# Kernel tuning notes

Measured on AMD Instinct MI355X. Metric: run time of the kernel, lower is better.

Reference implementation:

```python
import jax, jax.numpy as jnp
import numpy as np

B, L, D, H = 2, 2048, 2048, 16
Dh = D // H
EPS = 1e-6
THETA = 500000.0


def _rope_cos_sin(dh, seq_len):
    # matches init_rope: per-head dim, theta=500000
    inv_freqs = 1.0 / (THETA ** (jnp.arange(0, dh, 2, dtype=jnp.float32) / dh))  # [Dh/2]
    t = jnp.arange(seq_len, dtype=jnp.float32)
    freqs = jnp.outer(t, inv_freqs)  # [L, Dh/2]
    return jnp.cos(freqs), jnp.sin(freqs)


def _apply_rope(x, cos, sin):
    # x: [B,L,H,Dh]; cos/sin: [L,Dh/2]
    xr = x.reshape(*x.shape[:-1], -1, 2)  # [B,L,H,Dh/2,2]
    c = cos[None, :, None, :]
    s = sin[None, :, None, :]
    rot = jnp.stack([xr[..., 0] * c - xr[..., 1] * s,
                     xr[..., 1] * c + xr[..., 0] * s], axis=-1)
    return rot.reshape(x.shape)


def setup_inputs() -> dict:
    key = jax.random.key(0)
    ks = jax.random.split(key, 5)
    std = 0.02
    x = jax.random.normal(ks[0], (B, L, D), dtype=jnp.float32)
    Wq = std * jax.random.normal(ks[1], (D, H, Dh), dtype=jnp.float32)
    Wk = std * jax.random.normal(ks[2], (D, H, Dh), dtype=jnp.float32)
    Wv = std * jax.random.normal(ks[3], (D, H, Dh), dtype=jnp.float32)
    Wout = (std / jnp.sqrt(2.0 * 24)) * jax.random.normal(ks[4], (D, D), dtype=jnp.float32)
    attn_scale = jnp.asarray(jnp.log2(float(L) ** 2 - float(L)), dtype=jnp.float32)
    return {"x": x, "Wq": Wq, "Wk": Wk, "Wv": Wv, "Wout": Wout, "attn_scale": attn_scale}


def reference(x, Wq, Wk, Wv, Wout, attn_scale):
    cos, sin = _rope_cos_sin(Dh, L)
    q = jnp.einsum('bld,dhk->blhk', x, Wq)  # [B,L,H,Dh]
    k = jnp.einsum('bld,dhk->blhk', x, Wk)
    v = jnp.einsum('bld,dhk->blhk', x, Wv)
    q = _apply_rope(q, cos, sin)
    k = _apply_rope(k, cos, sin)
    # QK L2 normalization
    q = q / (jnp.linalg.norm(q, axis=-1, keepdims=True) + EPS)
    k = k / (jnp.linalg.norm(k, axis=-1, keepdims=True) + EPS)
    att = jnp.einsum('bqhd,bkhd->bhqk', q, k)  # [B,H,L,L]
    mask = jnp.tril(jnp.ones((1, 1, L, L), dtype=jnp.bool_))
    neg_inf = jnp.finfo(jnp.float32).min
    att = jnp.where(mask, att, neg_inf)
    att = attn_scale * att
    att = jax.nn.softmax(att, axis=-1)
    out = jnp.einsum('bhqk,bkhd->bqhd', att, v)  # [B,L,H,Dh]
    out = out.reshape(B, L, D)
    return jnp.einsum('bld,de->ble', out, Wout)
```

## Files before the change

kernel.cpp:

```cpp
#include <hip/hip_runtime.h>
#include <hip/hip_fp16.h>

#define B_ 2
#define L_ 2048
#define D_ 2048
#define H_ 16
#define DH_ 128

typedef _Float16 f16;
typedef _Float16 f16x8 __attribute__((ext_vector_type(8)));
typedef _Float16 f16x4 __attribute__((ext_vector_type(4)));
typedef _Float16 f16x2 __attribute__((ext_vector_type(2)));
typedef float f32x4 __attribute__((ext_vector_type(4)));

__device__ __forceinline__ void gload_lds16(const void* g, void* l) {
  __builtin_amdgcn_global_load_lds(
      (__attribute__((address_space(1))) void*)(void*)g,
      (__attribute__((address_space(3))) void*)l, 16, 0, 0);
}

template <int N>
__device__ __forceinline__ void waitcnt_vm() {
  if constexpr (N == 0) asm volatile("s_waitcnt vmcnt(0)" ::: "memory");
  else if constexpr (N == 4) asm volatile("s_waitcnt vmcnt(4)" ::: "memory");
  else if constexpr (N == 6) asm volatile("s_waitcnt vmcnt(6)" ::: "memory");
  else if constexpr (N == 8) asm volatile("s_waitcnt vmcnt(8)" ::: "memory");
}

__device__ __forceinline__ float rmax16(float v) {
  v = fmaxf(v, __shfl_xor(v, 1));
  v = fmaxf(v, __shfl_xor(v, 2));
  v = fmaxf(v, __shfl_xor(v, 4));
  v = fmaxf(v, __shfl_xor(v, 8));
  return v;
}
__device__ __forceinline__ float rsum16(float v) {
  v += __shfl_xor(v, 1);
  v += __shfl_xor(v, 2);
  v += __shfl_xor(v, 4);
  v += __shfl_xor(v, 8);
  return v;
}

__global__ __launch_bounds__(256) void k_cast(const float* __restrict__ in,
                                              f16* __restrict__ out, int n8) {
  int i = blockIdx.x * blockDim.x + threadIdx.x;
  if (i >= n8) return;
  const float4* p = (const float4*)in + (size_t)i * 2;
  float4 a = p[0], b = p[1];
  f16x8 o;
  o[0] = (f16)a.x; o[1] = (f16)a.y; o[2] = (f16)a.z; o[3] = (f16)a.w;
  o[4] = (f16)b.x; o[5] = (f16)b.y; o[6] = (f16)b.z; o[7] = (f16)b.w;
  *((f16x8*)out + i) = o;
}

__global__ __launch_bounds__(256) void k_transpose4(
    const float* __restrict__ W0, const float* __restrict__ W1,
    const float* __restrict__ W2, const float* __restrict__ W3,
    f16* __restrict__ T0, f16* __restrict__ T1, f16* __restrict__ T2,
    f16* __restrict__ T3) {
  int z = blockIdx.z;
  const float* src = (z == 0) ? W0 : (z == 1) ? W1 : (z == 2) ? W2 : W3;
  f16* dst = (z == 0) ? T0 : (z == 1) ? T1 : (z == 2) ? T2 : T3;
  __shared__ float tile[32][33];
  int tx = threadIdx.x, ty = threadIdx.y;
  int x = blockIdx.x * 32 + tx;
  int y0 = blockIdx.y * 32;
#pragma unroll
  for (int i = 0; i < 4; ++i)
    tile[ty + i * 8][tx] = src[(size_t)(y0 + ty + i * 8) * 2048 + x];
  __syncthreads();
  int ox = y0 + tx;
  int oy0 = blockIdx.x * 32;
#pragma unroll
  for (int i = 0; i < 4; ++i)
    dst[(size_t)(oy0 + ty + i * 8) * 2048 + ox] = (f16)tile[tx][ty + i * 8];
}


template <int NL>
__device__ __forceinline__ void stage_slot(const char* __restrict__ src,
                                           char* dst, int tid) {
#pragma unroll
  for (int j = 0; j < NL; ++j) {
    int ci = j * 512 + tid;
    int row = ci >> 3;
    int sc = (ci & 7) ^ (row & 7);
    gload_lds16(src + (size_t)row * 4096 + sc * 16, dst + ci * 16);
  }
}

template <int BM>
__device__ __forceinline__ void gemm8_core(const f16* __restrict__ A,
                                           const f16* __restrict__ BT,
                                           char* lds, int m0, int n0,
                                           f32x4 (&acc)[BM / 32][4]) {
  constexpr int WRS = BM / 2;
  constexpr int MR = BM / 32;
  constexpr int MPP = MR / 4;
  constexpr int ALOADS = BM / 128;
  constexpr int LPT = 2 * ALOADS + 4;
  constexpr int ABYTES = BM * 128;
  constexpr int BUFB = ABYTES + 32768;
  constexpr int nt = 32;

  const int tid = threadIdx.x;
  const int lane = tid & 63, w = tid >> 6;
  const int wr = w >> 2, wc = w & 3;
  const int li = lane & 15, lg = lane >> 4;

  const char* Ab = (const char*)A + (size_t)m0 * 4096;
  const char* Bb = (const char*)BT + (size_t)n0 * 4096;

  const int aoff0 = (wr * WRS + li) * 128 + ((lg) ^ (li & 7)) * 16;
  const int aoff1 = (wr * WRS + li) * 128 + ((4 + lg) ^ (li & 7)) * 16;
  const int boff0 = (wc * 64 + li) * 128 + ((lg) ^ (li & 7)) * 16;
  const int boff1 = (wc * 64 + li) * 128 + ((4 + lg) ^ (li & 7)) * 16;

#pragma unroll
  for (int t = 0; t < 2; ++t) {
    char* bA = lds + t * BUFB;
    stage_slot<ALOADS>(Ab + t * 128, bA, tid);
    stage_slot<ALOADS>(Ab + (size_t)WRS * 4096 + t * 128, bA + (size_t)WRS * 128, tid);
    stage_slot<2>(Bb + t * 128, bA + ABYTES, tid);
    stage_slot<2>(Bb + (size_t)128 * 4096 + t * 128, bA + ABYTES + 128 * 128, tid);
  }
  waitcnt_vm<LPT>();
  __builtin_amdgcn_s_barrier();

#pragma unroll 1
  for (int u = 0; u < nt; ++u) {
    const int c = u & 1;
    char* bufA = lds + c * BUFB;
    char* bufB = bufA + ABYTES;
    char* oA = lds + (c ^ 1) * BUFB;
    f16x8 bf[4][2];
#pragma unroll
    for (int p = 0; p < 4; ++p) {
      f16x8 af[MPP][2];
#pragma unroll
      for (int i = 0; i < MPP; ++i) {
        af[i][0] = *(const f16x8*)(bufA + aoff0 + (p * MPP + i) * 2048);
        af[i][1] = *(const f16x8*)(bufA + aoff1 + (p * MPP + i) * 2048);
      }
      if (p == 0) {
#pragma unroll
        for (int nc = 0; nc < 4; ++nc) {
          bf[nc][0] = *(const f16x8*)(bufB + boff0 + nc * 2048);
          bf[nc][1] = *(const f16x8*)(bufB + boff1 + nc * 2048);
        }
      }
      if (p == 0 && u >= 1 && u + 1 < nt)
        stage_slot<ALOADS>(Ab + (size_t)(u + 1) * 128, oA, tid);
      if (p == 1 && u >= 1 && u + 1 < nt)
        stage_slot<ALOADS>(Ab + (size_t)WRS * 4096 + (size_t)(u + 1) * 128,
                           oA + (size_t)WRS * 128, tid);
      if (p == 2 && u + 2 < nt)
        stage_slot<2>(Bb + (size_t)(u + 2) * 128, bufB, tid);
      if (p == 3 && u + 2 < nt)
        stage_slot<2>(Bb + (size_t)128 * 4096 + (size_t)(u + 2) * 128,
                      bufB + 128 * 128, tid);
      if (p == 3) {
        if (u + 2 < nt) waitcnt_vm<4>();
        else if (u + 1 < nt) waitcnt_vm<0>();
      }
      __builtin_amdgcn_s_barrier();
      asm volatile("s_waitcnt lgkmcnt(0)" ::: "memory");
      __builtin_amdgcn_sched_barrier(0);
      __builtin_amdgcn_s_setprio(1);
#pragma unroll
      for (int i = 0; i < MPP; ++i)
#pragma unroll
        for (int nc = 0; nc < 4; ++nc) {
          acc[p * MPP + i][nc] = __builtin_amdgcn_mfma_f32_16x16x32_f16(
              af[i][0], bf[nc][0], acc[p * MPP + i][nc], 0, 0, 0);
          acc[p * MPP + i][nc] = __builtin_amdgcn_mfma_f32_16x16x32_f16(
              af[i][1], bf[nc][1], acc[p * MPP + i][nc], 0, 0, 0);
        }
      __builtin_amdgcn_s_setprio(0);
      __builtin_amdgcn_s_barrier();
    }
  }
}

__global__ __launch_bounds__(512, 2) void k_gemm8_qkv(
    const f16* __restrict__ x16, const f16* __restrict__ WqT,
    const f16* __restrict__ WkT, const f16* __restrict__ WvT,
    f16* __restrict__ qh, f16* __restrict__ kh, f16* __restrict__ vTo) {
  __shared__ alignas(16) char lds[2 * (256 * 128 + 32768)];
  const int pb = blockIdx.x;
  const int lgc = (pb & 7) * 48 + (pb >> 3);
  const int z = lgc >> 7;
  const int r = lgc & 127;
  const int m0 = (r >> 3) * 256, n0 = (r & 7) * 256;
  const f16* BT = (z == 0) ? WqT : (z == 1) ? WkT : WvT;
  f32x4 acc[8][4] = {};
  gemm8_core<256>(x16, BT, lds, m0, n0, acc);

  const int lane = threadIdx.x & 63, w = threadIdx.x >> 6;
  const int wr = w >> 2, wc = w & 3, li = lane & 15, lg = lane >> 4;
  if (z < 2) {
    f16* out = (z == 0) ? qh : kh;
#pragma unroll
    for (int mr = 0; mr < 8; ++mr) {
      int mb = m0 + wr * 128 + mr * 16 + lg * 4;
#pragma unroll
      for (int nc = 0; nc < 4; ++nc) {
        int n = n0 + wc * 64 + nc * 16 + li;
        int h = n >> 7, dh = n & 127;
#pragma unroll
        for (int r2 = 0; r2 < 4; ++r2) {
          int m = mb + r2;
          int b = m >> 11, l = m & 2047;
          out[(((size_t)(b * 16 + h) * 2048 + l) << 7) + dh] = (f16)acc[mr][nc][r2];
        }
      }
    }
  } else {
#pragma unroll
    for (int mr = 0; mr < 8; ++mr) {
      int mb = m0 + wr * 128 + mr * 16 + lg * 4;
      int b = mb >> 11, l = mb & 2047;
#pragma unroll
      for (int nc = 0; nc < 4; ++nc) {
        int n = n0 + wc * 64 + nc * 16 + li;
        int h = n >> 7, dh = n & 127;
        f16x4 v4;
#pragma unroll
        for (int r2 = 0; r2 < 4; ++r2) v4[r2] = (f16)acc[mr][nc][r2];
        *(f16x4*)(vTo + ((size_t)(b * 16 + h) * 128 + dh) * 2048 + l) = v4;
      }
    }
  }
}

__global__ __launch_bounds__(512, 2) void k_gemm8_out(
    const f16* __restrict__ A, const f16* __restrict__ WoutT,
    float* __restrict__ out) {
  __shared__ alignas(16) char lds[2 * (128 * 128 + 32768)];
  const int pb = blockIdx.x;
  const int lgc = (pb & 7) * 32 + (pb >> 3);
  const int m0 = (lgc >> 3) * 128, n0 = (lgc & 7) * 256;
  f32x4 acc[4][4] = {};
  gemm8_core<128>(A, WoutT, lds, m0, n0, acc);

  const int lane = threadIdx.x & 63, w = threadIdx.x >> 6;
  const int wr = w >> 2, wc = w & 3, li = lane & 15, lg = lane >> 4;
#pragma unroll
  for (int mr = 0; mr < 4; ++mr) {
#pragma unroll
    for (int nc = 0; nc < 4; ++nc) {
      int n = n0 + wc * 64 + nc * 16 + li;
#pragma unroll
      for (int r2 = 0; r2 < 4; ++r2) {
        int m = m0 + wr * 64 + mr * 16 + lg * 4 + r2;
        out[(size_t)m * 2048 + n] = acc[mr][nc][r2];
      }
    }
  }
}

__global__ __launch_bounds__(256) void k_rope_norm(f16* __restrict__ qh,
                                                   f16* __restrict__ kh) {
  int gid = blockIdx.x * 4 + (threadIdx.x >> 6);
  int lane = threadIdx.x & 63;
  int which = gid >> 16;
  int r = gid & 65535;
  int l = r & 2047;
  f16* base = (which ? kh : qh) + (size_t)r * 128;
  f16x2 xv = *(f16x2*)(base + lane * 2);
  float x0 = (float)xv[0], x1 = (float)xv[1];
  float invf = exp2f(-(float)lane * 0.29580575889569f);
  float ang = (float)l * invf;
  float s, c;
  sincosf(ang, &s, &c);
  float y0 = x0 * c - x1 * s;
  float y1 = x1 * c + x0 * s;
  float ss = y0 * y0 + y1 * y1;
  ss += __shfl_xor(ss, 1);  ss += __shfl_xor(ss, 2);
  ss += __shfl_xor(ss, 4);  ss += __shfl_xor(ss, 8);
  ss += __shfl_xor(ss, 16); ss += __shfl_xor(ss, 32);
  float inv = 1.0f / (sqrtf(ss) + 1e-6f);
  f16x2 o;
  o[0] = (f16)(y0 * inv);
  o[1] = (f16)(y1 * inv);
  *(f16x2*)(base + lane * 2) = o;
}

__global__ __launch_bounds__(256) void k_flash(
    const f16* __restrict__ qh, const f16* __restrict__ kh,
    const f16* __restrict__ vT, f16* __restrict__ attO,
    const float* __restrict__ ascale_p) {
  const int bh = blockIdx.y;
  const int tid = threadIdx.x, lane = tid & 63, w = tid >> 6;
  const int li = lane & 15, lg = lane >> 4;
  const float csc = ascale_p[0] * 1.44269504088896f;
  const float thr = 8.0f / csc;

  __shared__ alignas(16) f16 Ks[64 * 136];
  __shared__ alignas(16) f16 Vs[128 * 72];
  __shared__ alignas(16) f16 Ps[4][16 * 72];

  const f16* qb = qh + (size_t)bh * 2048 * 128;
  const f16* kb = kh + (size_t)bh * 2048 * 128;
  const f16* vb = vT + (size_t)bh * 128 * 2048;
  const int b = bh >> 4, h = bh & 15;

#pragma unroll 1
  for (int ti = 0; ti < 2; ++ti) {
    const int t = ti ? (31 - (int)blockIdx.x) : (int)blockIdx.x;
    const int qw = t * 64 + w * 16;

    f16x8 Qr[4];
#pragma unroll
    for (int ks = 0; ks < 4; ++ks)
      Qr[ks] = *(const f16x8*)(qb + (size_t)(qw + li) * 128 + ks * 32 + lg * 8);

    f32x4 Oa[8] = {};
    float mrow[4], lrow[4];
#pragma unroll
    for (int r = 0; r < 4; ++r) { mrow[r] = -1e30f; lrow[r] = 0.0f; }

#pragma unroll 1
    for (int kt = 0; kt <= t; ++kt) {
      const int k0 = kt * 64;
      __syncthreads();
#pragma unroll
      for (int p = 0; p < 4; ++p) {
        int e = (p * 256 + tid) * 8;
        int row = e >> 7, col = e & 127;
        *(f16x8*)(Ks + row * 136 + col) =
            *(const f16x8*)(kb + (size_t)(k0 + row) * 128 + col);
        int row2 = e >> 6, col2 = e & 63;
        *(f16x8*)(Vs + row2 * 72 + col2) =
            *(const f16x8*)(vb + (size_t)row2 * 2048 + k0 + col2);
      }
      __syncthreads();

      f32x4 Sa[4] = {};
      __builtin_amdgcn_s_setprio(1);
#pragma unroll
      for (int ks = 0; ks < 4; ++ks) {
        f16x8 kf4[4];
#pragma unroll
        for (int kf = 0; kf < 4; ++kf)
          kf4[kf] = *(const f16x8*)(Ks + (kf * 16 + li) * 136 + ks * 32 + lg * 8);
#pragma unroll
        for (int kf = 0; kf < 4; ++kf)
          Sa[kf] = __builtin_amdgcn_mfma_f32_16x16x32_f16(Qr[ks], kf4[kf],
                                                          Sa[kf], 0, 0, 0);
      }
      __builtin_amdgcn_s_setprio(0);

      if (kt == t) {
#pragma unroll
        for (int kf = 0; kf < 4; ++kf)
#pragma unroll
          for (int r = 0; r < 4; ++r) {
            int qq = qw + lg * 4 + r;
            int kk = k0 + kf * 16 + li;
            if (kk > qq) Sa[kf][r] = -1e30f;
          }
      }

      float vmax[4];
      bool need = false;
#pragma unroll
      for (int r = 0; r < 4; ++r) {
        float v = fmaxf(fmaxf(Sa[0][r], Sa[1][r]), fmaxf(Sa[2][r], Sa[3][r]));
        v = rmax16(v);
        vmax[r] = v;
        need |= (v > mrow[r] + thr);
      }
      if (__any(need)) {
#pragma unroll
        for (int r = 0; r < 4; ++r) {
          float mnew = fmaxf(mrow[r], vmax[r]);
          float sc = exp2f(csc * (mrow[r] - mnew));
          mrow[r] = mnew;
          lrow[r] *= sc;
#pragma unroll
          for (int df = 0; df < 8; ++df) Oa[df][r] *= sc;
        }
      }
#pragma unroll
      for (int r = 0; r < 4; ++r) {
        float rs = 0.0f;
#pragma unroll
        for (int kf = 0; kf < 4; ++kf) {
          float p = exp2f(csc * (Sa[kf][r] - mrow[r]));
          Sa[kf][r] = p;
          rs += p;
        }
        rs = rsum16(rs);
        lrow[r] += rs;
      }

      f16* Pw = &Ps[w][0];
#pragma unroll
      for (int kf = 0; kf < 4; ++kf)
#pragma unroll
        for (int r = 0; r < 4; ++r)
          Pw[(lg * 4 + r) * 72 + kf * 16 + li] = (f16)Sa[kf][r];
      asm volatile("s_waitcnt lgkmcnt(0)" ::: "memory");
      __builtin_amdgcn_sched_barrier(0);
      __builtin_amdgcn_s_setprio(1);
#pragma unroll
      for (int k2 = 0; k2 < 2; ++k2) {
        f16x8 pa, vfr[8];
        pa = *(const f16x8*)(Pw + li * 72 + k2 * 32 + lg * 8);
#pragma unroll
        for (int df = 0; df < 8; ++df)
          vfr[df] = *(const f16x8*)(Vs + (df * 16 + li) * 72 + k2 * 32 + lg * 8);
#pragma unroll
        for (int df = 0; df < 8; ++df)
          Oa[df] = __builtin_amdgcn_mfma_f32_16x16x32_f16(pa, vfr[df],
                                                          Oa[df], 0, 0, 0);
      }
      __builtin_amdgcn_s_setprio(0);
    }

#pragma unroll
    for (int r = 0; r < 4; ++r) {
      float inv = 1.0f / lrow[r];
      int q = qw + lg * 4 + r;
      f16* orow = attO + (size_t)(b * 2048 + q) * 2048 + h * 128;
#pragma unroll
      for (int df = 0; df < 8; ++df)
        orow[df * 16 + li] = (f16)(Oa[df][r] * inv);
    }
  }
}

extern "C" void kernel_launch(void* const* d_in, const int* in_sizes, int n_in,
                              void* d_out, int out_size, void* d_ws, size_t ws_size,
                              hipStream_t stream) {
  (void)in_sizes; (void)n_in; (void)out_size; (void)ws_size;
  const float* x = (const float*)d_in[0];
  const float* Wq = (const float*)d_in[1];
  const float* Wk = (const float*)d_in[2];
  const float* Wv = (const float*)d_in[3];
  const float* Wout = (const float*)d_in[4];
  const float* ascale = (const float*)d_in[5];

  char* ws = (char*)d_ws;
  f16* x16 = (f16*)(ws);
  f16* WoutT = (f16*)(ws + (16ull << 20));
  f16* WqT = (f16*)(ws + (24ull << 20));
  f16* WkT = (f16*)(ws + (32ull << 20));
  f16* WvT = (f16*)(ws + (40ull << 20));
  f16* qh = (f16*)(ws + (48ull << 20));
  f16* kh = (f16*)(ws + (64ull << 20));
  f16* vT = (f16*)(ws + (80ull << 20));
  f16* attO = (f16*)(ws + (24ull << 20));

  k_cast<<<dim3(4096), dim3(256), 0, stream>>>(x, x16, 1048576);
  k_transpose4<<<dim3(64, 64, 4), dim3(32, 8), 0, stream>>>(Wq, Wk, Wv, Wout,
                                                            WqT, WkT, WvT, WoutT);
  k_gemm8_qkv<<<dim3(384), dim3(512), 0, stream>>>(x16, WqT, WkT, WvT, qh, kh, vT);
  k_rope_norm<<<dim3(32768), dim3(256), 0, stream>>>(qh, kh);
  k_flash<<<dim3(16, 32), dim3(256), 0, stream>>>(qh, kh, vT, attO, ascale);
  k_gemm8_out<<<dim3(256), dim3(512), 0, stream>>>(attO, WoutT, (float*)d_out);
}
```

Measured before the change: 435.6 us.

## Fuse QKV GEMM into one wide-N kernel and double-buffer flash K/V tiles

The QKV projection becomes a single GEMM over the concatenated WqT|WkT|WvT weights, using 128x384 tiles and 512 blocks. It relies on WqT, WkT and WvT sitting contiguously in the workspace at 8MB strides. The flash attention kernel now stages K/V tiles with async global-to-LDS loads into double buffers using XOR swizzles instead of padded rows, so the next tile loads while the current one is computed. This removes the synchronous load-then-sync stall per key tile. The cost is more LDS use and a three-phase MFMA schedule with extra barriers in the GEMM.

Result: faster. 423.9 us (-2.7%).

```diff
diff --git a/kernel.cpp b/kernel.cpp
--- a/kernel.cpp
+++ b/kernel.cpp
@@ -77,7 +77,6 @@
     dst[(size_t)(oy0 + ty + i * 8) * 2048 + ox] = (f16)tile[tx][ty + i * 8];
 }
 
-
 template <int NL>
 __device__ __forceinline__ void stage_slot(const char* __restrict__ src,
                                            char* dst, int tid) {
@@ -87,6 +86,145 @@
     int row = ci >> 3;
     int sc = (ci & 7) ^ (row & 7);
     gload_lds16(src + (size_t)row * 4096 + sc * 16, dst + ci * 16);
+  }
+}
+
+__global__ __launch_bounds__(512, 2) void k_gemm8_qkv(
+    const f16* __restrict__ x16, const f16* __restrict__ WT ,
+    f16* __restrict__ qh, f16* __restrict__ kh, f16* __restrict__ vTo) {
+  constexpr int ABYTES = 128 * 128;
+  constexpr int BUFB = ABYTES + 384 * 128;
+  constexpr int nt = 32;
+  __shared__ alignas(16) char lds[2 * BUFB];
+
+  const int pb = blockIdx.x;
+  const int lgc = (pb & 7) * 64 + (pb >> 3);
+  const int m0 = (lgc >> 4) * 128;
+  const int n0 = (lgc & 15) * 384;
+
+  const int tid = threadIdx.x;
+  const int lane = tid & 63, w = tid >> 6;
+  const int wr = w >> 2, wc = w & 3;
+  const int li = lane & 15, lg = lane >> 4;
+
+  const char* Ab = (const char*)x16 + (size_t)m0 * 4096;
+  const char* Bb = (const char*)WT + (size_t)n0 * 4096;
+
+  f32x4 acc[4][6] = {};
+
+#pragma unroll
+  for (int t = 0; t < 2; ++t) {
+    char* bA = lds + t * BUFB;
+    stage_slot<2>(Ab + t * 128, bA, tid);
+    stage_slot<6>(Bb + t * 128, bA + ABYTES, tid);
+  }
+  waitcnt_vm<8>();
+  __builtin_amdgcn_s_barrier();
+
+  const int sx = (li & 7);
+
+#pragma unroll 1
+  for (int u = 0; u < nt; ++u) {
+    const int c = u & 1;
+    char* bufA = lds + c * BUFB;
+    char* bufB = bufA + ABYTES;
+    char* oA = lds + (c ^ 1) * BUFB;
+    f16x8 af[4][2], bf[6][2];
+
+#pragma unroll
+    for (int mr = 0; mr < 4; ++mr) {
+      int rb = (wr * 64 + mr * 16 + li) * 128;
+      af[mr][0] = *(const f16x8*)(bufA + rb + ((lg ^ sx) << 4));
+      af[mr][1] = *(const f16x8*)(bufA + rb + (((4 + lg) ^ sx) << 4));
+    }
+#pragma unroll
+    for (int nc = 0; nc < 2; ++nc) {
+      int rb = (wc * 96 + nc * 16 + li) * 128;
+      bf[nc][0] = *(const f16x8*)(bufB + rb + ((lg ^ sx) << 4));
+      bf[nc][1] = *(const f16x8*)(bufB + rb + (((4 + lg) ^ sx) << 4));
+    }
+    if (u >= 1 && u + 1 < nt) stage_slot<2>(Ab + (size_t)(u + 1) * 128, oA, tid);
+    __builtin_amdgcn_s_barrier();
+    asm volatile("s_waitcnt lgkmcnt(0)" ::: "memory");
+    __builtin_amdgcn_sched_barrier(0);
+    __builtin_amdgcn_s_setprio(1);
+#pragma unroll
+    for (int mr = 0; mr < 4; ++mr)
+#pragma unroll
+      for (int nc = 0; nc < 2; ++nc) {
+        acc[mr][nc] = __builtin_amdgcn_mfma_f32_16x16x32_f16(af[mr][0], bf[nc][0],
+                                                             acc[mr][nc], 0, 0, 0);
+        acc[mr][nc] = __builtin_amdgcn_mfma_f32_16x16x32_f16(af[mr][1], bf[nc][1],
+                                                             acc[mr][nc], 0, 0, 0);
+      }
+    __builtin_amdgcn_s_setprio(0);
+    __builtin_amdgcn_s_barrier();
+
+#pragma unroll
+    for (int nc = 2; nc < 6; ++nc) {
+      int rb = (wc * 96 + nc * 16 + li) * 128;
+      bf[nc][0] = *(const f16x8*)(bufB + rb + ((lg ^ sx) << 4));
+      bf[nc][1] = *(const f16x8*)(bufB + rb + (((4 + lg) ^ sx) << 4));
+    }
+    __builtin_amdgcn_s_barrier();
+    asm volatile("s_waitcnt lgkmcnt(0)" ::: "memory");
+    __builtin_amdgcn_sched_barrier(0);
+    __builtin_amdgcn_s_setprio(1);
+#pragma unroll
+    for (int mr = 0; mr < 4; ++mr)
+#pragma unroll
+      for (int nc = 2; nc < 4; ++nc) {
+        acc[mr][nc] = __builtin_amdgcn_mfma_f32_16x16x32_f16(af[mr][0], bf[nc][0],
+                                                             acc[mr][nc], 0, 0, 0);
+        acc[mr][nc] = __builtin_amdgcn_mfma_f32_16x16x32_f16(af[mr][1], bf[nc][1],
+                                                             acc[mr][nc], 0, 0, 0);
+      }
+    __builtin_amdgcn_s_setprio(0);
+    __builtin_amdgcn_s_barrier();
+
+    if (u + 2 < nt) stage_slot<6>(Bb + (size_t)(u + 2) * 128, bufB, tid);
+    if (u + 2 < nt) waitcnt_vm<6>();
+    else if (u + 1 < nt) waitcnt_vm<0>();
+    __builtin_amdgcn_s_barrier();
+    __builtin_amdgcn_sched_barrier(0);
+    __builtin_amdgcn_s_setprio(1);
+#pragma unroll
+    for (int mr = 0; mr < 4; ++mr)
+#pragma unroll
+      for (int nc = 4; nc < 6; ++nc) {
+        acc[mr][nc] = __builtin_amdgcn_mfma_f32_16x16x32_f16(af[mr][0], bf[nc][0],
+                                                             acc[mr][nc], 0, 0, 0);
+        acc[mr][nc] = __builtin_amdgcn_mfma_f32_16x16x32_f16(af[mr][1], bf[nc][1],
+                                                             acc[mr][nc], 0, 0, 0);
+      }
+    __builtin_amdgcn_s_setprio(0);
+    __builtin_amdgcn_s_barrier();
+  }
+
+#pragma unroll
+  for (int mr = 0; mr < 4; ++mr) {
+    int mb = m0 + wr * 64 + mr * 16 + lg * 4;
+    int b = mb >> 11, l = mb & 2047;
+#pragma unroll
+    for (int nc = 0; nc < 6; ++nc) {
+      int n = n0 + wc * 96 + nc * 16 + li;
+      int z = n >> 11, n2 = n & 2047;
+      int h = n2 >> 7, dh = n2 & 127;
+      if (z < 2) {
+        f16* out = (z == 0) ? qh : kh;
+#pragma unroll
+        for (int r2 = 0; r2 < 4; ++r2) {
+          int m = mb + r2;
+          out[(((size_t)(b * 16 + h) * 2048 + (m & 2047)) << 7) + dh] =
+              (f16)acc[mr][nc][r2];
+        }
+      } else {
+        f16x4 v4;
+#pragma unroll
+        for (int r2 = 0; r2 < 4; ++r2) v4[r2] = (f16)acc[mr][nc][r2];
+        *(f16x4*)(vTo + ((size_t)(b * 16 + h) * 128 + dh) * 2048 + l) = v4;
+      }
+    }
   }
 }
 
@@ -179,57 +317,6 @@
         }
       __builtin_amdgcn_s_setprio(0);
       __builtin_amdgcn_s_barrier();
-    }
-  }
-}
-
-__global__ __launch_bounds__(512, 2) void k_gemm8_qkv(
-    const f16* __restrict__ x16, const f16* __restrict__ WqT,
-    const f16* __restrict__ WkT, const f16* __restrict__ WvT,
-    f16* __restrict__ qh, f16* __restrict__ kh, f16* __restrict__ vTo) {
-  __shared__ alignas(16) char lds[2 * (256 * 128 + 32768)];
-  const int pb = blockIdx.x;
-  const int lgc = (pb & 7) * 48 + (pb >> 3);
-  const int z = lgc >> 7;
-  const int r = lgc & 127;
-  const int m0 = (r >> 3) * 256, n0 = (r & 7) * 256;
-  const f16* BT = (z == 0) ? WqT : (z == 1) ? WkT : WvT;
-  f32x4 acc[8][4] = {};
-  gemm8_core<256>(x16, BT, lds, m0, n0, acc);
-
-  const int lane = threadIdx.x & 63, w = threadIdx.x >> 6;
-  const int wr = w >> 2, wc = w & 3, li = lane & 15, lg = lane >> 4;
-  if (z < 2) {
-    f16* out = (z == 0) ? qh : kh;
-#pragma unroll
-    for (int mr = 0; mr < 8; ++mr) {
-      int mb = m0 + wr * 128 + mr * 16 + lg * 4;
-#pragma unroll
-      for (int nc = 0; nc < 4; ++nc) {
-        int n = n0 + wc * 64 + nc * 16 + li;
-        int h = n >> 7, dh = n & 127;
-#pragma unroll
-        for (int r2 = 0; r2 < 4; ++r2) {
-          int m = mb + r2;
-          int b = m >> 11, l = m & 2047;
-          out[(((size_t)(b * 16 + h) * 2048 + l) << 7) + dh] = (f16)acc[mr][nc][r2];
-        }
-      }
-    }
-  } else {
-#pragma unroll
-    for (int mr = 0; mr < 8; ++mr) {
-      int mb = m0 + wr * 128 + mr * 16 + lg * 4;
-      int b = mb >> 11, l = mb & 2047;
-#pragma unroll
-      for (int nc = 0; nc < 4; ++nc) {
-        int n = n0 + wc * 64 + nc * 16 + li;
-        int h = n >> 7, dh = n & 127;
-        f16x4 v4;
-#pragma unroll
-        for (int r2 = 0; r2 < 4; ++r2) v4[r2] = (f16)acc[mr][nc][r2];
-        *(f16x4*)(vTo + ((size_t)(b * 16 + h) * 128 + dh) * 2048 + l) = v4;
-      }
     }
   }
 }
@@ -297,14 +384,30 @@
   const float csc = ascale_p[0] * 1.44269504088896f;
   const float thr = 8.0f / csc;
 
-  __shared__ alignas(16) f16 Ks[64 * 136];
-  __shared__ alignas(16) f16 Vs[128 * 72];
+  __shared__ alignas(16) f16 Ks[2][64 * 128];
+  __shared__ alignas(16) f16 Vs[2][128 * 64];
   __shared__ alignas(16) f16 Ps[4][16 * 72];
 
   const f16* qb = qh + (size_t)bh * 2048 * 128;
-  const f16* kb = kh + (size_t)bh * 2048 * 128;
-  const f16* vb = vT + (size_t)bh * 128 * 2048;
+  const char* kbB = (const char*)(kh + (size_t)bh * 2048 * 128);
+  const char* vbB = (const char*)(vT + (size_t)bh * 128 * 2048);
   const int b = bh >> 4, h = bh & 15;
+  const int sx = li & 7;
+
+  auto stage_tile = [&](int kt, int bsel) {
+    char* Kd = (char*)Ks[bsel];
+    char* Vd = (char*)Vs[bsel];
+    const char* ksrc = kbB + (size_t)kt * 64 * 256;
+    const char* vsrc = vbB + (size_t)kt * 128;
+#pragma unroll
+    for (int j = 0; j < 4; ++j) {
+      int ci = j * 256 + tid;
+      int row = ci >> 4, sc = (ci & 15) ^ (row & 7);
+      gload_lds16(ksrc + (size_t)row * 256 + sc * 16, Kd + ci * 16);
+      int row2 = ci >> 3, sc2 = (ci & 7) ^ (row2 & 7);
+      gload_lds16(vsrc + (size_t)row2 * 4096 + sc2 * 16, Vd + ci * 16);
+    }
+  };
 
 #pragma unroll 1
   for (int ti = 0; ti < 2; ++ti) {
@@ -321,21 +424,16 @@
 #pragma unroll
     for (int r = 0; r < 4; ++r) { mrow[r] = -1e30f; lrow[r] = 0.0f; }
 
+    stage_tile(0, 0);
+    waitcnt_vm<0>();
+    __syncthreads();
+
 #pragma unroll 1
     for (int kt = 0; kt <= t; ++kt) {
-      const int k0 = kt * 64;
-      __syncthreads();
-#pragma unroll
-      for (int p = 0; p < 4; ++p) {
-        int e = (p * 256 + tid) * 8;
-        int row = e >> 7, col = e & 127;
-        *(f16x8*)(Ks + row * 136 + col) =
-            *(const f16x8*)(kb + (size_t)(k0 + row) * 128 + col);
-        int row2 = e >> 6, col2 = e & 63;
-        *(f16x8*)(Vs + row2 * 72 + col2) =
-            *(const f16x8*)(vb + (size_t)row2 * 2048 + k0 + col2);
-      }
-      __syncthreads();
+      const int c = kt & 1;
+      if (kt + 1 <= t) stage_tile(kt + 1, c ^ 1);
+      const char* Kb = (const char*)Ks[c];
+      const char* Vb = (const char*)Vs[c];
 
       f32x4 Sa[4] = {};
       __builtin_amdgcn_s_setprio(1);
@@ -343,8 +441,10 @@
       for (int ks = 0; ks < 4; ++ks) {
         f16x8 kf4[4];
 #pragma unroll
-        for (int kf = 0; kf < 4; ++kf)
-          kf4[kf] = *(const f16x8*)(Ks + (kf * 16 + li) * 136 + ks * 32 + lg * 8);
+        for (int kf = 0; kf < 4; ++kf) {
+          int cc = (ks * 4 + lg) ^ sx;
+          kf4[kf] = *(const f16x8*)(Kb + (kf * 16 + li) * 256 + cc * 16);
+        }
 #pragma unroll
         for (int kf = 0; kf < 4; ++kf)
           Sa[kf] = __builtin_amdgcn_mfma_f32_16x16x32_f16(Qr[ks], kf4[kf],
@@ -358,7 +458,7 @@
 #pragma unroll
           for (int r = 0; r < 4; ++r) {
             int qq = qw + lg * 4 + r;
-            int kk = k0 + kf * 16 + li;
+            int kk = t * 64 + kf * 16 + li;
             if (kk > qq) Sa[kf][r] = -1e30f;
           }
       }
@@ -410,14 +510,18 @@
         f16x8 pa, vfr[8];
         pa = *(const f16x8*)(Pw + li * 72 + k2 * 32 + lg * 8);
 #pragma unroll
-        for (int df = 0; df < 8; ++df)
-          vfr[df] = *(const f16x8*)(Vs + (df * 16 + li) * 72 + k2 * 32 + lg * 8);
+        for (int df = 0; df < 8; ++df) {
+          int cc = (k2 * 4 + lg) ^ sx;
+          vfr[df] = *(const f16x8*)(Vb + (df * 16 + li) * 128 + cc * 16);
+        }
 #pragma unroll
         for (int df = 0; df < 8; ++df)
           Oa[df] = __builtin_amdgcn_mfma_f32_16x16x32_f16(pa, vfr[df],
                                                           Oa[df], 0, 0, 0);
       }
       __builtin_amdgcn_s_setprio(0);
+      waitcnt_vm<0>();
+      __syncthreads();
     }
 
 #pragma unroll
@@ -429,6 +533,7 @@
       for (int df = 0; df < 8; ++df)
         orow[df * 16 + li] = (f16)(Oa[df][r] * inv);
     }
+    __syncthreads();
   }
 }
 
@@ -457,7 +562,7 @@
   k_cast<<<dim3(4096), dim3(256), 0, stream>>>(x, x16, 1048576);
   k_transpose4<<<dim3(64, 64, 4), dim3(32, 8), 0, stream>>>(Wq, Wk, Wv, Wout,
                                                             WqT, WkT, WvT, WoutT);
-  k_gemm8_qkv<<<dim3(384), dim3(512), 0, stream>>>(x16, WqT, WkT, WvT, qh, kh, vT);
+  k_gemm8_qkv<<<dim3(512), dim3(512), 0, stream>>>(x16, WqT, qh, kh, vT);
   k_rope_norm<<<dim3(32768), dim3(256), 0, stream>>>(qh, kh);
   k_flash<<<dim3(16, 32), dim3(256), 0, stream>>>(qh, kh, vT, attO, ascale);
   k_gemm8_out<<<dim3(256), dim3(512), 0, stream>>>(attO, WoutT, (float*)d_out);
```
